# Kernel optimization log

Measured on AMD Instinct MI355X. Metric: run time of the kernel, lower is better.

The kernel has to match this reference:

```python
import math
import jax, jax.numpy as jnp
import numpy as np

NUM_HEADS = 16
EPS = 1e-6


def _rotate_half(t):
    t1, t2 = jnp.split(t, 2, axis=-1)
    return jnp.concatenate([-t2, t1], axis=-1)


def _rmsnorm(t, w):
    # compute in fp32 like the torch module, then cast back and apply affine
    x32 = t.astype(jnp.float32)
    r = jax.lax.rsqrt(jnp.mean(x32 * x32, axis=-1, keepdims=True) + EPS)
    return (x32 * r).astype(t.dtype) * w


def setup_inputs() -> dict:
    key = jax.random.key(0)
    ks = jax.random.split(key, 12)
    B, N, C, T = 8, 1024, 1024, 1024
    hd2 = (C // NUM_HEADS) // 2  # 32
    inp = {
        "x": jax.random.normal(ks[0], (B, N, C), jnp.float32),
        "temb": jax.random.normal(ks[1], (B, T), jnp.float32),
        "cos_y": jax.random.uniform(ks[2], (1, 1, N, hd2), jnp.float32, -1.0, 1.0),
        "sin_y": jax.random.uniform(ks[3], (1, 1, N, hd2), jnp.float32, -1.0, 1.0),
        "cos_x": jax.random.uniform(ks[4], (1, 1, N, hd2), jnp.float32, -1.0, 1.0),
        "sin_x": jax.random.uniform(ks[5], (1, 1, N, hd2), jnp.float32, -1.0, 1.0),
        # params; weights stored (in, out) so y = x @ W + b (== torch x @ W.T)
        "Wqkv": jax.random.normal(ks[6], (C, 3 * C), jnp.float32) * 0.02,
        "bqkv": jnp.zeros((3 * C,), jnp.float32),
        "Wt": jax.random.normal(ks[7], (T, 3 * C), jnp.float32) * 0.02,
        "bt": jnp.zeros((3 * C,), jnp.float32),
        "Wp": jax.random.normal(ks[8], (C, C), jnp.float32) * 0.02,
        "bp": jnp.zeros((C,), jnp.float32),
        "qn_w": jnp.ones((C // NUM_HEADS,), jnp.float32),
        "kn_w": jnp.ones((C // NUM_HEADS,), jnp.float32),
    }
    return inp


def reference(x, temb, cos_y, sin_y, cos_x, sin_x,
              Wqkv, bqkv, Wt, bt, Wp, bp, qn_w, kn_w):
    B, N, C = x.shape
    H = NUM_HEADS
    hd = C // H
    # fused QKV projection + additive time conditioning
    qkv = x @ Wqkv + bqkv + (temb @ Wt + bt)[:, None, :]         # [B,N,3C]
    qkv = qkv.reshape(B, N, 3, H, hd).transpose(2, 0, 3, 1, 4)    # [3,B,H,N,hd]
    q, k, v = qkv[0], qkv[1], qkv[2]
    # per-head QK RMSNorm with affine
    q = _rmsnorm(q, qn_w)
    k = _rmsnorm(k, kn_w)
    # axial 2D RoPE on the y-half and x-half of head_dim
    qy, qx = jnp.split(q, 2, axis=-1)
    ky, kx = jnp.split(k, 2, axis=-1)
    qy = qy * cos_y + _rotate_half(qy) * sin_y
    ky = ky * cos_y + _rotate_half(ky) * sin_y
    qx = qx * cos_x + _rotate_half(qx) * sin_x
    kx = kx * cos_x + _rotate_half(kx) * sin_x
    q = jnp.concatenate([qy, qx], axis=-1)
    k = jnp.concatenate([ky, kx], axis=-1)
    # scaled dot-product attention (no dropout at eval)
    scale = 1.0 / math.sqrt(hd)
    scores = jnp.einsum('bhqd,bhkd->bhqk', q, k) * scale
    attn = jax.nn.softmax(scores, axis=-1)
    out = jnp.einsum('bhqk,bhkd->bhqd', attn, v)                  # [B,H,N,hd]
    out = out.transpose(0, 2, 1, 3).reshape(B, N, C)
    return out @ Wp + bp
```

## Files before the change

kernel.cpp:

```cpp
#include <hip/hip_runtime.h>
#include <cstdint>

typedef unsigned short u16;
typedef __bf16 bf16x8 __attribute__((ext_vector_type(8)));
typedef float f32x4 __attribute__((ext_vector_type(4)));

__device__ __forceinline__ u16 f2bf(float f) {
  __bf16 h = (__bf16)f;
  return __builtin_bit_cast(u16, h);
}
__device__ __forceinline__ float bf2f(u16 u) {
  union { uint32_t u; float f; } v; v.u = ((uint32_t)u) << 16;
  return v.f;
}

__device__ __forceinline__ void gload16(const void* g, const void* l) {
  __builtin_amdgcn_global_load_lds(
      (const __attribute__((address_space(1))) uint32_t*)(uintptr_t)g,
      (__attribute__((address_space(3))) uint32_t*)(uintptr_t)l, 16, 0, 0);
}

__device__ __forceinline__ f32x4 mfma16(bf16x8 a, bf16x8 b, f32x4 c) {
  return __builtin_amdgcn_mfma_f32_16x16x32_bf16(a, b, c, 0, 0, 0);
}

__device__ __forceinline__ int swz(int row, int col) {
  return row * 64 + ((((col >> 3) ^ (row & 7)) << 3) | (col & 7));
}

__global__ __launch_bounds__(256)
void k_cvt(const float* __restrict__ src, u16* __restrict__ dst, int n4) {
  int i = blockIdx.x * 256 + threadIdx.x;
  if (i >= n4) return;
  float4 v = ((const float4*)src)[i];
  union { u16 s[4]; uint2 u; } o;
  o.s[0] = f2bf(v.x); o.s[1] = f2bf(v.y); o.s[2] = f2bf(v.z); o.s[3] = f2bf(v.w);
  ((uint2*)dst)[i] = o.u;
}

__global__ __launch_bounds__(256)
void k_transpose(const float* __restrict__ src, u16* __restrict__ dst, int R, int Cc) {
  __shared__ u16 t[64 * 66];
  int r0 = blockIdx.y * 64, c0 = blockIdx.x * 64;
  #pragma unroll
  for (int i = 0; i < 16; i++) {
    int e = i * 256 + threadIdx.x;
    int rl = e >> 6, cl = e & 63;
    t[cl * 66 + rl] = f2bf(src[(size_t)(r0 + rl) * Cc + c0 + cl]);
  }
  __syncthreads();
  #pragma unroll
  for (int i = 0; i < 16; i++) {
    int e = i * 256 + threadIdx.x;
    int ro = e >> 6, co = e & 63;
    dst[(size_t)(c0 + ro) * R + r0 + co] = t[ro * 66 + co];
  }
}

__global__ __launch_bounds__(256)
void k_temb_part(const float* __restrict__ temb, const float* __restrict__ Wt,
                 float* __restrict__ part) {
  const int j = blockIdx.x * 256 + threadIdx.x;
  const int k0 = blockIdx.y * 32;
  float acc[8];
  #pragma unroll
  for (int b = 0; b < 8; b++) acc[b] = 0.f;
  #pragma unroll 4
  for (int k = k0; k < k0 + 32; k++) {
    float wv = Wt[(size_t)k * 3072 + j];
    #pragma unroll
    for (int b = 0; b < 8; b++) acc[b] += temb[b * 1024 + k] * wv;
  }
  float* p = part + (size_t)blockIdx.y * 24576 + j;
  #pragma unroll
  for (int b = 0; b < 8; b++) p[b * 3072] = acc[b];
}

__global__ __launch_bounds__(256)
void k_temb_red(const float* __restrict__ part, const float* __restrict__ bt,
                const float* __restrict__ bqkv, float* __restrict__ tcomb) {
  const int j = blockIdx.x * 256 + threadIdx.x;
  const int b = blockIdx.y;
  const float* p = part + b * 3072 + j;
  float a = bt[j] + bqkv[j];
  #pragma unroll
  for (int kt = 0; kt < 32; kt++) a += p[(size_t)kt * 24576];
  tcomb[b * 3072 + j] = a;
}

template <int MODE>
__global__ __launch_bounds__(512, 2)
void k_gemm(const u16* __restrict__ A, const u16* __restrict__ Bt,
            u16* __restrict__ outb, float* __restrict__ outf,
            const float* __restrict__ bias, int K, int Ntot) {
  __shared__ __align__(16) u16 As[3][128 * 64];
  __shared__ __align__(16) u16 Bs[3][256 * 64];

  const int nb = (int)gridDim.x;
  const int chunk = nb >> 3;
  const int bid = (int)blockIdx.x;
  const int sb = (bid & 7) * chunk + (bid >> 3);
  const int NBN = Ntot >> 8;
  const int m0 = (sb / NBN) * 128;
  const int n0 = (sb % NBN) * 256;

  const int lane = threadIdx.x & 63;
  const int w = threadIdx.x >> 6;
  const int wm = w >> 2;
  const int wn = w & 3;
  const int l15 = lane & 15;
  const int g8 = (lane >> 4) * 8;

  const int srow = lane >> 3;
  const int schunk = ((lane & 7) ^ srow) * 8;
  const u16* Ag = A + (size_t)(m0 + w * 16 + srow) * K + schunk;
  const u16* Bg = Bt + (size_t)(n0 + w * 32 + srow) * K + schunk;

  f32x4 acc[4][4];
  #pragma unroll
  for (int i = 0; i < 4; i++)
    #pragma unroll
    for (int j = 0; j < 4; j++) acc[i][j] = (f32x4){0.f, 0.f, 0.f, 0.f};

  auto stage = [&](int kt_, int buf_) {
    const int ko = kt_ << 6;
    #pragma unroll
    for (int tt = 0; tt < 2; tt++)
      gload16(Ag + (size_t)(tt * 8) * K + ko, &As[buf_][(w * 2 + tt) * 512]);
    #pragma unroll
    for (int tt = 0; tt < 4; tt++)
      gload16(Bg + (size_t)(tt * 8) * K + ko, &Bs[buf_][(w * 4 + tt) * 512]);
  };

  const int NT = K >> 6;
  stage(0, 0);
  stage(1, 1);

  int cur = 0;
  for (int kt = 0; kt < NT; kt++) {
    if (kt + 1 < NT) asm volatile("s_waitcnt vmcnt(6)" ::: "memory");
    else             asm volatile("s_waitcnt vmcnt(0)" ::: "memory");
    __builtin_amdgcn_s_barrier();
    __builtin_amdgcn_sched_barrier(0);
    if (kt + 2 < NT) stage(kt + 2, cur + 2 >= 3 ? cur - 1 : cur + 2);

    bf16x8 af[2][4], bfr[2][4];
    #pragma unroll
    for (int s = 0; s < 2; s++) {
      #pragma unroll
      for (int mf = 0; mf < 4; mf++)
        af[s][mf] = *(const bf16x8*)&As[cur][swz(wm * 64 + mf * 16 + l15, s * 32 + g8)];
      #pragma unroll
      for (int nf = 0; nf < 4; nf++)
        bfr[s][nf] = *(const bf16x8*)&Bs[cur][swz(wn * 64 + nf * 16 + l15, s * 32 + g8)];
    }
    __builtin_amdgcn_s_setprio(1);
    #pragma unroll
    for (int mf = 0; mf < 4; mf++)
      #pragma unroll
      for (int nf = 0; nf < 4; nf++) {
        acc[mf][nf] = mfma16(af[0][mf], bfr[0][nf], acc[mf][nf]);
        acc[mf][nf] = mfma16(af[1][mf], bfr[1][nf], acc[mf][nf]);
      }
    __builtin_amdgcn_s_setprio(0);
    cur = cur + 1 >= 3 ? 0 : cur + 1;
  }

  const int rl = (lane >> 4) * 4;
  #pragma unroll
  for (int mf = 0; mf < 4; mf++) {
    #pragma unroll
    for (int nf = 0; nf < 4; nf++) {
      #pragma unroll
      for (int r = 0; r < 4; r++) {
        int grow = m0 + wm * 64 + mf * 16 + rl + r;
        int gcol = n0 + wn * 64 + nf * 16 + l15;
        float v = acc[mf][nf][r];
        if (MODE == 0) {
          int b = grow >> 10;
          v += bias[b * Ntot + gcol];
          outb[(size_t)grow * Ntot + gcol] = f2bf(v);
        } else {
          v += bias[gcol];
          outf[(size_t)grow * Ntot + gcol] = v;
        }
      }
    }
  }
}

__global__ __launch_bounds__(256)
void k_rrv(const u16* __restrict__ qkv,
           const float* __restrict__ cos_y, const float* __restrict__ sin_y,
           const float* __restrict__ cos_x, const float* __restrict__ sin_x,
           const float* __restrict__ qn_w, const float* __restrict__ kn_w,
           u16* __restrict__ Qo, u16* __restrict__ Ko, u16* __restrict__ VT) {
  __shared__ u16 t[64 * 68];
  const int n0 = blockIdx.x * 64, h = blockIdx.y, b = blockIdx.z;
  const int bh = b * 16 + h;
  const int lane = threadIdx.x & 63, w = threadIdx.x >> 6;
  const int l15 = lane & 15, lg = lane >> 4;
  float4 qw = *(const float4*)(qn_w + l15 * 4);
  float4 kw = *(const float4*)(kn_w + l15 * 4);
  const float sgn = (lane & 4) ? 1.0f : -1.0f;
  const float* ct = (lane & 8) ? cos_x : cos_y;
  const float* st = (lane & 8) ? sin_x : sin_y;
  const float QSCALE = 0.18033688011112042f;

  #pragma unroll
  for (int rr = 0; rr < 4; rr++) {
    int row = n0 + w * 16 + rr * 4 + lg;
    size_t src = (size_t)(b * 1024 + row) * 3072 + h * 64 + l15 * 4;
    uint2 qu = *(const uint2*)(qkv + src);
    uint2 ku = *(const uint2*)(qkv + src + 1024);
    float q[4], k[4];
    q[0] = bf2f((u16)qu.x); q[1] = bf2f((u16)(qu.x >> 16));
    q[2] = bf2f((u16)qu.y); q[3] = bf2f((u16)(qu.y >> 16));
    k[0] = bf2f((u16)ku.x); k[1] = bf2f((u16)(ku.x >> 16));
    k[2] = bf2f((u16)ku.y); k[3] = bf2f((u16)(ku.y >> 16));
    float sq = q[0]*q[0] + q[1]*q[1] + q[2]*q[2] + q[3]*q[3];
    float sk = k[0]*k[0] + k[1]*k[1] + k[2]*k[2] + k[3]*k[3];
    #pragma unroll
    for (int m = 1; m < 16; m <<= 1) {
      sq += __shfl_xor(sq, m);
      sk += __shfl_xor(sk, m);
    }
    float rq = rsqrtf(sq * (1.0f / 64.0f) + 1e-6f);
    float rk = rsqrtf(sk * (1.0f / 64.0f) + 1e-6f);
    float4 cc = *(const float4*)(ct + (size_t)row * 32 + (lane & 7) * 4);
    float4 ss = *(const float4*)(st + (size_t)row * 32 + (lane & 7) * 4);
    float qn[4], kn[4];
    qn[0] = q[0]*rq*qw.x; qn[1] = q[1]*rq*qw.y; qn[2] = q[2]*rq*qw.z; qn[3] = q[3]*rq*qw.w;
    kn[0] = k[0]*rk*kw.x; kn[1] = k[1]*rk*kw.y; kn[2] = k[2]*rk*kw.z; kn[3] = k[3]*rk*kw.w;
    float c[4] = {cc.x, cc.y, cc.z, cc.w};
    float s[4] = {ss.x, ss.y, ss.z, ss.w};
    union { u16 e[4]; uint2 u; } oq, ok;
    #pragma unroll
    for (int j = 0; j < 4; j++) {
      float qp = __shfl_xor(qn[j], 4);
      float kp = __shfl_xor(kn[j], 4);
      oq.e[j] = f2bf((qn[j] * c[j] + sgn * qp * s[j]) * QSCALE);
      ok.e[j] = f2bf(kn[j] * c[j] + sgn * kp * s[j]);
    }
    size_t dst = ((size_t)bh * 1024 + row) * 64 + l15 * 4;
    *(uint2*)(Qo + dst) = oq.u;
    *(uint2*)(Ko + dst) = ok.u;
  }

  #pragma unroll
  for (int i = 0; i < 4; i++) {
    int e = i * 256 + threadIdx.x;
    int n = e >> 4, dc = e & 15;
    uint2 v = *(const uint2*)(qkv + (size_t)(b * 1024 + n0 + n) * 3072 + 2048 + h * 64 + dc * 4);
    t[(dc * 4 + 0) * 68 + n] = (u16)v.x;
    t[(dc * 4 + 1) * 68 + n] = (u16)(v.x >> 16);
    t[(dc * 4 + 2) * 68 + n] = (u16)v.y;
    t[(dc * 4 + 3) * 68 + n] = (u16)(v.y >> 16);
  }
  __syncthreads();
  #pragma unroll
  for (int i = 0; i < 4; i++) {
    int e = i * 256 + threadIdx.x;
    int d = e >> 4, nc = e & 15;
    const u16* p = &t[d * 68 + nc * 4];
    uint2 o;
    o.x = (uint32_t)p[0] | ((uint32_t)p[1] << 16);
    o.y = (uint32_t)p[2] | ((uint32_t)p[3] << 16);
    *(uint2*)(VT + ((size_t)bh * 64 + d) * 1024 + n0 + nc * 4) = o;
  }
}

__global__ __launch_bounds__(256, 2)
void k_attn(const u16* __restrict__ Q, const u16* __restrict__ Kb,
            const u16* __restrict__ VT, u16* __restrict__ Ob) {
  __shared__ u16 Ks[2][4096], VTs[2][4096], Ps[4][2048];
  const int lane = threadIdx.x & 63;
  const int w = threadIdx.x >> 6;
  const int bh = blockIdx.x;
  const int qt = blockIdx.y;
  const int b = bh >> 4, h = bh & 15;
  const size_t base = (size_t)bh * 65536;
  const int q0 = qt * 128;
  const int scol = ((lane & 7) ^ (lane >> 3)) * 8;
  const int lr = lane >> 3;

  bf16x8 aq[2][2];
  #pragma unroll
  for (int i = 0; i < 2; i++)
    #pragma unroll
    for (int s = 0; s < 2; s++)
      aq[i][s] = *(const bf16x8*)(Q + base +
          (size_t)(q0 + w * 32 + i * 16 + (lane & 15)) * 64 + s * 32 + (lane >> 4) * 8);

  f32x4 acc_o[2][4];
  float lpar[2][4];
  #pragma unroll
  for (int i = 0; i < 2; i++)
    #pragma unroll
    for (int r = 0; r < 4; r++) {
      acc_o[i][r] = (f32x4){0.f, 0.f, 0.f, 0.f};
      lpar[i][r] = 0.f;
    }

  #pragma unroll
  for (int tt = 0; tt < 2; tt++) {
    int t = w * 2 + tt;
    gload16(Kb + base + (size_t)(8 * t + lr) * 64 + scol, &Ks[0][t * 512]);
    gload16(VT + base + (size_t)(8 * t + lr) * 1024 + scol, &VTs[0][t * 512]);
  }

  for (int it = 0; it < 16; it++) {
    __syncthreads();
    const int cur = it & 1;
    if (it < 15) {
      const int nxt = cur ^ 1;
      const int j1 = (it + 1) * 64;
      #pragma unroll
      for (int tt = 0; tt < 2; tt++) {
        int t = w * 2 + tt;
        gload16(Kb + base + (size_t)(j1 + 8 * t + lr) * 64 + scol, &Ks[nxt][t * 512]);
        gload16(VT + base + (size_t)(8 * t + lr) * 1024 + j1 + scol, &VTs[nxt][t * 512]);
      }
    }
    const u16* K_ = Ks[cur];
    const u16* V_ = VTs[cur];

    f32x4 accs[2][4];
    #pragma unroll
    for (int i = 0; i < 2; i++)
      #pragma unroll
      for (int nt = 0; nt < 4; nt++) accs[i][nt] = (f32x4){0.f, 0.f, 0.f, 0.f};
    #pragma unroll
    for (int s = 0; s < 2; s++) {
      bf16x8 bk[4];
      #pragma unroll
      for (int nt = 0; nt < 4; nt++)
        bk[nt] = *(const bf16x8*)&K_[swz(nt * 16 + (lane & 15), s * 32 + (lane >> 4) * 8)];
      #pragma unroll
      for (int i = 0; i < 2; i++)
        #pragma unroll
        for (int nt = 0; nt < 4; nt++)
          accs[i][nt] = mfma16(aq[i][s], bk[nt], accs[i][nt]);
    }

    #pragma unroll
    for (int i = 0; i < 2; i++) {
      #pragma unroll
      for (int nt = 0; nt < 4; nt++) {
        #pragma unroll
        for (int r = 0; r < 4; r++) {
          float p = __builtin_amdgcn_exp2f(accs[i][nt][r]);
          lpar[i][r] += p;
          Ps[w][swz(i * 16 + (lane >> 4) * 4 + r, nt * 16 + (lane & 15))] = f2bf(p);
        }
      }
    }
    asm volatile("s_waitcnt lgkmcnt(0)" ::: "memory");

    #pragma unroll
    for (int s = 0; s < 2; s++) {
      bf16x8 bv[4];
      #pragma unroll
      for (int dt = 0; dt < 4; dt++)
        bv[dt] = *(const bf16x8*)&V_[swz(dt * 16 + (lane & 15), s * 32 + (lane >> 4) * 8)];
      #pragma unroll
      for (int i = 0; i < 2; i++) {
        bf16x8 ap = *(const bf16x8*)&Ps[w][swz(i * 16 + (lane & 15), s * 32 + (lane >> 4) * 8)];
        #pragma unroll
        for (int dt = 0; dt < 4; dt++)
          acc_o[i][dt] = mfma16(ap, bv[dt], acc_o[i][dt]);
      }
    }
  }

  #pragma unroll
  for (int i = 0; i < 2; i++) {
    float inv[4];
    #pragma unroll
    for (int r = 0; r < 4; r++) {
      float l = lpar[i][r];
      #pragma unroll
      for (int m = 1; m < 16; m <<= 1) l += __shfl_xor(l, m);
      inv[r] = 1.0f / l;
    }
    #pragma unroll
    for (int dt = 0; dt < 4; dt++)
      #pragma unroll
      for (int r = 0; r < 4; r++) {
        int row = q0 + w * 32 + i * 16 + (lane >> 4) * 4 + r;
        int col = h * 64 + dt * 16 + (lane & 15);
        Ob[((size_t)b * 1024 + row) * 1024 + col] = f2bf(acc_o[i][dt][r] * inv[r]);
      }
  }
}

extern "C" void kernel_launch(void* const* d_in, const int* in_sizes, int n_in,
                              void* d_out, int out_size, void* d_ws, size_t ws_size,
                              hipStream_t stream) {
  const float* x     = (const float*)d_in[0];
  const float* temb  = (const float*)d_in[1];
  const float* cos_y = (const float*)d_in[2];
  const float* sin_y = (const float*)d_in[3];
  const float* cos_x = (const float*)d_in[4];
  const float* sin_x = (const float*)d_in[5];
  const float* Wqkv  = (const float*)d_in[6];
  const float* bqkv  = (const float*)d_in[7];
  const float* Wt    = (const float*)d_in[8];
  const float* bt    = (const float*)d_in[9];
  const float* Wp    = (const float*)d_in[10];
  const float* bp    = (const float*)d_in[11];
  const float* qn_w  = (const float*)d_in[12];
  const float* kn_w  = (const float*)d_in[13];
  float* out = (float*)d_out;

  char* ws = (char*)d_ws;
  u16*   x_bf  = (u16*)(ws);
  u16*   WqkvT = (u16*)(ws + 16777216);
  u16*   WpT   = (u16*)(ws + 23068672);
  float* tcomb = (float*)(ws + 25165824);
  u16*   qkv   = (u16*)(ws + 25264128);
  u16*   Qb    = (u16*)(ws + 75595776);
  u16*   Kb    = (u16*)(ws + 92372992);
  u16*   VTb   = (u16*)(ws + 109150208);
  float* tpart = (float*)(ws + 125927424);
  u16*   att   = x_bf;

  k_cvt<<<8192, 256, 0, stream>>>(x, x_bf, 8192 * 1024 / 4);
  k_transpose<<<dim3(48, 16), 256, 0, stream>>>(Wqkv, WqkvT, 1024, 3072);
  k_transpose<<<dim3(16, 16), 256, 0, stream>>>(Wp, WpT, 1024, 1024);
  k_temb_part<<<dim3(12, 32), 256, 0, stream>>>(temb, Wt, tpart);
  k_temb_red<<<dim3(12, 8), 256, 0, stream>>>(tpart, bt, bqkv, tcomb);
  k_gemm<0><<<dim3(768), 512, 0, stream>>>(x_bf, WqkvT, qkv, nullptr, tcomb, 1024, 3072);
  k_rrv<<<dim3(16, 16, 8), 256, 0, stream>>>(qkv, cos_y, sin_y, cos_x, sin_x,
                                             qn_w, kn_w, Qb, Kb, VTb);
  k_attn<<<dim3(128, 8), 256, 0, stream>>>(Qb, Kb, VTb, att);
  k_gemm<1><<<dim3(256), 512, 0, stream>>>(att, WpT, nullptr, out, bp, 1024, 1024);
}
```

Before: 299.4 us.

## Split GEMM k-step into two half-phases interleaving B-tile loads with MFMA

Restructures the GEMM main loop so each k-iteration runs as two phases. Phase one loads the A tile and the low half of the B tile, then phase two loads the high half of B, each followed by MFMAs on the matching half of the output columns. Prefetch issue and barriers are spread across the two phases to overlap LDS reads and global loads with compute in a finer-grained ping-pong. This adds a second barrier per iteration and more complex vmcnt accounting, which risks extra synchronisation stalls.

```diff
diff --git a/kernel.cpp b/kernel.cpp
--- a/kernel.cpp
+++ b/kernel.cpp
@@ -97,9 +97,8 @@
   __shared__ __align__(16) u16 Bs[3][256 * 64];
 
   const int nb = (int)gridDim.x;
-  const int chunk = nb >> 3;
   const int bid = (int)blockIdx.x;
-  const int sb = (bid & 7) * chunk + (bid >> 3);
+  const int sb = (bid & 7) * (nb >> 3) + (bid >> 3);
   const int NBN = Ntot >> 8;
   const int m0 = (sb / NBN) * 128;
   const int n0 = (sb % NBN) * 256;
@@ -110,11 +109,11 @@
   const int wn = w & 3;
   const int l15 = lane & 15;
   const int g8 = (lane >> 4) * 8;
-
-  const int srow = lane >> 3;
-  const int schunk = ((lane & 7) ^ srow) * 8;
-  const u16* Ag = A + (size_t)(m0 + w * 16 + srow) * K + schunk;
-  const u16* Bg = Bt + (size_t)(n0 + w * 32 + srow) * K + schunk;
+  const int lr = lane >> 3;
+  const int schunk = ((lane & 7) ^ lr) * 8;
+
+  const u16* Ag = A + (size_t)(m0 + w * 16 + lr) * K + schunk;
+  const u16* Bg = Bt + (size_t)(n0 + lr) * K + schunk;
 
   f32x4 acc[4][4];
   #pragma unroll
@@ -122,47 +121,88 @@
     #pragma unroll
     for (int j = 0; j < 4; j++) acc[i][j] = (f32x4){0.f, 0.f, 0.f, 0.f};
 
-  auto stage = [&](int kt_, int buf_) {
+  auto stageA_Blo = [&](int kt_, int buf_) {
     const int ko = kt_ << 6;
     #pragma unroll
-    for (int tt = 0; tt < 2; tt++)
-      gload16(Ag + (size_t)(tt * 8) * K + ko, &As[buf_][(w * 2 + tt) * 512]);
-    #pragma unroll
-    for (int tt = 0; tt < 4; tt++)
-      gload16(Bg + (size_t)(tt * 8) * K + ko, &Bs[buf_][(w * 4 + tt) * 512]);
+    for (int t = 0; t < 2; t++) {
+      int r0 = w * 16 + t * 8;
+      gload16(Ag + (size_t)(t * 8) * K + ko, &As[buf_][r0 * 64]);
+    }
+    #pragma unroll
+    for (int t = 0; t < 2; t++) {
+      int f0 = w * 16 + t * 8;
+      int r0 = (f0 >> 5) * 64 + (f0 & 31);
+      gload16(Bg + (size_t)r0 * K + ko, &Bs[buf_][r0 * 64]);
+    }
   };
+  auto stageBhi = [&](int kt_, int buf_) {
+    const int ko = kt_ << 6;
+    #pragma unroll
+    for (int t = 0; t < 2; t++) {
+      int f0 = w * 16 + t * 8;
+      int r0 = (f0 >> 5) * 64 + 32 + (f0 & 31);
+      gload16(Bg + (size_t)r0 * K + ko, &Bs[buf_][r0 * 64]);
+    }
+  };
 
   const int NT = K >> 6;
-  stage(0, 0);
-  stage(1, 1);
+  stageA_Blo(0, 0); stageBhi(0, 0);
+  stageA_Blo(1, 1); stageBhi(1, 1);
+  asm volatile("s_waitcnt vmcnt(8)" ::: "memory");
+  __builtin_amdgcn_s_barrier();
+  asm volatile("" ::: "memory");
 
   int cur = 0;
   for (int kt = 0; kt < NT; kt++) {
-    if (kt + 1 < NT) asm volatile("s_waitcnt vmcnt(6)" ::: "memory");
-    else             asm volatile("s_waitcnt vmcnt(0)" ::: "memory");
-    __builtin_amdgcn_s_barrier();
-    __builtin_amdgcn_sched_barrier(0);
-    if (kt + 2 < NT) stage(kt + 2, cur + 2 >= 3 ? cur - 1 : cur + 2);
+    const int nxtbuf = cur + 2 >= 3 ? cur - 1 : cur + 2;
 
     bf16x8 af[2][4], bfr[2][4];
     #pragma unroll
-    for (int s = 0; s < 2; s++) {
+    for (int s = 0; s < 2; s++)
       #pragma unroll
       for (int mf = 0; mf < 4; mf++)
         af[s][mf] = *(const bf16x8*)&As[cur][swz(wm * 64 + mf * 16 + l15, s * 32 + g8)];
-      #pragma unroll
-      for (int nf = 0; nf < 4; nf++)
+    #pragma unroll
+    for (int s = 0; s < 2; s++)
+      #pragma unroll
+      for (int nf = 0; nf < 2; nf++)
         bfr[s][nf] = *(const bf16x8*)&Bs[cur][swz(wn * 64 + nf * 16 + l15, s * 32 + g8)];
-    }
+    if (kt + 2 < NT) stageA_Blo(kt + 2, nxtbuf);
+    if (kt <= NT - 2) asm volatile("s_waitcnt vmcnt(6)" ::: "memory");
+    else              asm volatile("s_waitcnt vmcnt(0)" ::: "memory");
+    __builtin_amdgcn_s_barrier();
+    asm volatile("" ::: "memory");
     __builtin_amdgcn_s_setprio(1);
     #pragma unroll
-    for (int mf = 0; mf < 4; mf++)
-      #pragma unroll
-      for (int nf = 0; nf < 4; nf++) {
-        acc[mf][nf] = mfma16(af[0][mf], bfr[0][nf], acc[mf][nf]);
-        acc[mf][nf] = mfma16(af[1][mf], bfr[1][nf], acc[mf][nf]);
-      }
+    for (int s = 0; s < 2; s++)
+      #pragma unroll
+      for (int mf = 0; mf < 4; mf++)
+        #pragma unroll
+        for (int nf = 0; nf < 2; nf++)
+          acc[mf][nf] = mfma16(af[s][mf], bfr[s][nf], acc[mf][nf]);
     __builtin_amdgcn_s_setprio(0);
+
+    #pragma unroll
+    for (int s = 0; s < 2; s++)
+      #pragma unroll
+      for (int nf = 2; nf < 4; nf++)
+        bfr[s][nf] = *(const bf16x8*)&Bs[cur][swz(wn * 64 + nf * 16 + l15, s * 32 + g8)];
+    if (kt + 2 < NT) stageBhi(kt + 2, nxtbuf);
+    if (kt < NT - 2)       asm volatile("s_waitcnt vmcnt(6)" ::: "memory");
+    else if (kt == NT - 2) asm volatile("s_waitcnt vmcnt(2)" ::: "memory");
+    else                   asm volatile("s_waitcnt vmcnt(0)" ::: "memory");
+    __builtin_amdgcn_s_barrier();
+    asm volatile("" ::: "memory");
+    __builtin_amdgcn_s_setprio(1);
+    #pragma unroll
+    for (int s = 0; s < 2; s++)
+      #pragma unroll
+      for (int mf = 0; mf < 4; mf++)
+        #pragma unroll
+        for (int nf = 2; nf < 4; nf++)
+          acc[mf][nf] = mfma16(af[s][mf], bfr[s][nf], acc[mf][nf]);
+    __builtin_amdgcn_s_setprio(0);
+
     cur = cur + 1 >= 3 ? 0 : cur + 1;
   }
 
```

Measured after the change: 284.0 us. 1.05x faster.
